# Kernel tuning notes

Hardware: AMD Instinct MI355X
Metric: run time of the kernel (lower is better)

Reference implementation:

```python
import jax, jax.numpy as jnp
import numpy as np


def setup_inputs() -> dict:
    key = jax.random.key(0)
    k1, k2, k3, k4 = jax.random.split(key, 4)
    B, T, C, H = 4, 4096, 1024, 64
    x = jax.random.normal(k1, (B, T, C), dtype=jnp.float32)
    Wq = jax.random.normal(k2, (C, H), dtype=jnp.float32) * (C ** -0.5)
    Wk = jax.random.normal(k3, (C, H), dtype=jnp.float32) * (C ** -0.5)
    Wv = jax.random.normal(k4, (C, H), dtype=jnp.float32) * (C ** -0.5)
    return {"x": x, "Wq": Wq, "Wk": Wk, "Wv": Wv}


def reference(x, Wq, Wk, Wv):
    B, T, C = x.shape
    q = jnp.einsum('btc,ch->bth', x, Wq)  # [B,T,H]
    k = jnp.einsum('btc,ch->bth', x, Wk)
    v = jnp.einsum('btc,ch->bth', x, Wv)
    # NOTE: original scales by C**0.5 (embed_dim), not head_size**0.5
    scale = jnp.asarray(C, x.dtype) ** 0.5
    wei = jnp.einsum('bth,bsh->bts', q, k) / scale  # [B,T,T]
    causal = jnp.tril(jnp.ones((T, T), dtype=bool))
    wei = jnp.where(causal, wei, -jnp.inf)
    wei = jax.nn.softmax(wei, axis=-1)  # dropout p=0.0 -> identity
    return jnp.einsum('bts,bsh->bth', wei, v)  # [B,T,H]
```

## Files before the change

### kernel.cpp

```cpp
#include <hip/hip_runtime.h>
#include <hip/hip_bf16.h>

typedef __bf16 bf16;
typedef __bf16 bf16x8 __attribute__((ext_vector_type(8)));
typedef __bf16 bf16x4 __attribute__((ext_vector_type(4)));
typedef float  f32x4  __attribute__((ext_vector_type(4)));

#define MFMA16(A, B, C) __builtin_amdgcn_mfma_f32_16x16x32_bf16((A), (B), (C), 0, 0, 0)

static constexpr int Bn = 4;
static constexpr int T  = 4096;
static constexpr int Cd = 1024;
static constexpr int H  = 64;
static constexpr int NG = 192;
static constexpr int CH = 8;
static constexpr int SLOTS_PER_B = 288;
static constexpr float QSCALE = 0.03125f;

__device__ inline void dma16(const void* g, void* l) {
    __builtin_amdgcn_global_load_lds(
        (const __attribute__((address_space(1))) unsigned int*)g,
        (__attribute__((address_space(3))) unsigned int*)l, 16, 0, 0);
}

__device__ inline bf16x8 cvt_bf16x8(float4 a, float4 b) {
    bf16x8 r;
    r[0] = (bf16)a.x; r[1] = (bf16)a.y; r[2] = (bf16)a.z; r[3] = (bf16)a.w;
    r[4] = (bf16)b.x; r[5] = (bf16)b.y; r[6] = (bf16)b.z; r[7] = (bf16)b.w;
    return r;
}

__global__ __launch_bounds__(256) void wt_kernel(const float* __restrict__ Wq,
                                                 const float* __restrict__ Wk,
                                                 const float* __restrict__ Wv,
                                                 bf16* __restrict__ Wt) {
    __shared__ float s[64][65];
    const int cb = blockIdx.x;
    const int m  = blockIdx.y;
    const float* W = (m == 0) ? Wq : (m == 1) ? Wk : Wv;
    for (int i = threadIdx.x; i < 64 * 64; i += 256) {
        const int c = i >> 6, h = i & 63;
        s[c][h] = W[(cb * 64 + c) * H + h];
    }
    __syncthreads();
    for (int i = threadIdx.x; i < 64 * 64; i += 256) {
        const int n = i >> 6, c = i & 63;
        Wt[(m * 64 + n) * Cd + cb * 64 + c] = (bf16)s[c][n];
    }
}

__global__ __launch_bounds__(256, 4) void proj_kernel(const float* __restrict__ x,
                                                      const bf16* __restrict__ Wt,
                                                      bf16* __restrict__ qw,
                                                      bf16* __restrict__ kw,
                                                      bf16* __restrict__ vtw) {
    const int tid  = threadIdx.x;
    const int lane = tid & 63;
    const int w    = tid >> 6;
    const int ml   = lane & 15;
    const int quad = lane >> 4;

    const long r0 = (long)blockIdx.x * 16;

    __shared__ float sX[2][16][64];

    const int drow = w * 4 + (lane >> 4);
    const int dchk = lane & 15;
    const float* gx = x + (r0 + drow) * Cd + ((dchk ^ drow) << 2);

    f32x4 acc[3];
    #pragma unroll
    for (int j = 0; j < 3; ++j) acc[j] = f32x4{0.f, 0.f, 0.f, 0.f};

    const bf16* wb = Wt + (long)(w * 48 + ml) * Cd + quad * 8;

    dma16(gx, &sX[0][w * 4][0]);
    __syncthreads();

    int buf = 0;
    for (int kb = 0; kb < Cd; kb += 64) {
        if (kb + 64 < Cd)
            dma16(gx + kb + 64, &sX[buf ^ 1][w * 4][0]);

        const bf16x8 w00 = *(const bf16x8*)(wb + kb);
        const bf16x8 w01 = *(const bf16x8*)(wb + 16 * Cd + kb);
        const bf16x8 w02 = *(const bf16x8*)(wb + 32 * Cd + kb);
        const bf16x8 w10 = *(const bf16x8*)(wb + kb + 32);
        const bf16x8 w11 = *(const bf16x8*)(wb + 16 * Cd + kb + 32);
        const bf16x8 w12 = *(const bf16x8*)(wb + 32 * Cd + kb + 32);

        const int c00 = (0 * 8 + quad * 2) ^ ml;
        const int c10 = (1 * 8 + quad * 2) ^ ml;
        const float4 lo0 = *(const float4*)&sX[buf][ml][c00 << 2];
        const float4 hi0 = *(const float4*)&sX[buf][ml][(c00 ^ 1) << 2];
        const float4 lo1 = *(const float4*)&sX[buf][ml][c10 << 2];
        const float4 hi1 = *(const float4*)&sX[buf][ml][(c10 ^ 1) << 2];
        const bf16x8 af0 = cvt_bf16x8(lo0, hi0);
        const bf16x8 af1 = cvt_bf16x8(lo1, hi1);

        acc[0] = MFMA16(af0, w00, acc[0]);
        acc[1] = MFMA16(af0, w01, acc[1]);
        acc[2] = MFMA16(af0, w02, acc[2]);
        acc[0] = MFMA16(af1, w10, acc[0]);
        acc[1] = MFMA16(af1, w11, acc[1]);
        acc[2] = MFMA16(af1, w12, acc[2]);

        __syncthreads();
        buf ^= 1;
    }

    const int b = (int)(r0 >> 12);
    const long rowb = r0 + quad * 4;
    const int  tloc = (int)(rowb & 4095);

    #pragma unroll
    for (int f = 0; f < 3; ++f) {
        const int base = w * 48 + f * 16;
        const int sel  = base >> 6;
        const int h    = (base & 63) + ml;
        if (sel == 0) {
            #pragma unroll
            for (int rr = 0; rr < 4; ++rr)
                qw[(rowb + rr) * H + h] = (bf16)(acc[f][rr] * QSCALE);
        } else if (sel == 1) {
            #pragma unroll
            for (int rr = 0; rr < 4; ++rr)
                kw[(rowb + rr) * H + h] = (bf16)acc[f][rr];
        } else {
            bf16x4 pv;
            #pragma unroll
            for (int rr = 0; rr < 4; ++rr) pv[rr] = (bf16)acc[f][rr];
            *(bf16x4*)(vtw + ((long)(b * H + h)) * T + tloc) = pv;
        }
    }
}

__global__ __launch_bounds__(256, 3) void attn_kernel(const bf16* __restrict__ qw,
                                                      const bf16* __restrict__ kw,
                                                      const bf16* __restrict__ vtw,
                                                      float* __restrict__ pO,
                                                      float* __restrict__ pL) {
    const int qt = blockIdx.x;
    const int c  = blockIdx.y;
    const int b  = blockIdx.z;
    const int g  = qt >> 3, r = qt & 7;
    if (c > g) return;

    const int tid  = threadIdx.x;
    const int lane = tid & 63;
    const int w    = tid >> 6;
    const int ml   = lane & 15;
    const int quad = lane >> 4;
    const int mx   = ml & 7;

    __shared__ bf16 sK[2][64][64];
    __shared__ bf16 sVt[2][64][64];
    __shared__ bf16 sP[4][16][72];

    const int t0 = qt * 64;

    const bf16* q0 = qw + ((long)b * T + t0 + w * 16 + ml) * H;
    const bf16x8 aq0 = *(const bf16x8*)(q0 + quad * 8);
    const bf16x8 aq1 = *(const bf16x8*)(q0 + 32 + quad * 8);

    f32x4 O[4];
    #pragma unroll
    for (int ht = 0; ht < 4; ++ht) O[ht] = f32x4{0.f, 0.f, 0.f, 0.f};
    float lrow[4] = {0.f, 0.f, 0.f, 0.f};

    const int trow = t0 + w * 16 + quad * 4;
    const int jt0 = c * CH;
    const int jt1 = (c == g) ? qt + 1 : (c + 1) * CH;

    const int drow = w * 8 + (lane >> 3);
    const int dsw  = ((lane & 7) ^ (drow & 7)) << 3;
    const bf16* kbase = kw + (long)b * T * H;
    const bf16* vbase = vtw + (long)b * H * T;
    const long koffA = (long)drow * H + dsw;
    const long koffB = koffA + 32 * H;
    const long voffA = (long)drow * T + dsw;
    const long voffB = voffA + (long)32 * T;

    {
        const long ks0 = (long)jt0 * 64;
        dma16(kbase + ks0 * H + koffA, &sK[0][w * 8][0]);
        dma16(kbase + ks0 * H + koffB, &sK[0][32 + w * 8][0]);
        dma16(vbase + ks0 + voffA, &sVt[0][w * 8][0]);
        dma16(vbase + ks0 + voffB, &sVt[0][32 + w * 8][0]);
    }
    __syncthreads();

    int buf = 0;
    for (int jt = jt0; jt < jt1; ++jt) {
        if (jt + 1 < jt1) {
            const long ksn = (long)(jt + 1) * 64;
            dma16(kbase + ksn * H + koffA, &sK[buf ^ 1][w * 8][0]);
            dma16(kbase + ksn * H + koffB, &sK[buf ^ 1][32 + w * 8][0]);
            dma16(vbase + ksn + voffA, &sVt[buf ^ 1][w * 8][0]);
            dma16(vbase + ksn + voffB, &sVt[buf ^ 1][32 + w * 8][0]);
        }

        const int s0 = jt * 64;
        const bool diag = (jt == qt);
        #pragma unroll
        for (int nt = 0; nt < 4; ++nt) {
            f32x4 sacc = f32x4{0.f, 0.f, 0.f, 0.f};
            sacc = MFMA16(aq0, *(const bf16x8*)&sK[buf][nt * 16 + ml][(quad ^ mx) << 3], sacc);
            sacc = MFMA16(aq1, *(const bf16x8*)&sK[buf][nt * 16 + ml][((4 + quad) ^ mx) << 3], sacc);
            const int col = s0 + nt * 16 + ml;
            #pragma unroll
            for (int rr = 0; rr < 4; ++rr) {
                const float p = (diag && col > trow + rr) ? 0.f : __expf(sacc[rr]);
                lrow[rr] += p;
                sP[w][quad * 4 + rr][nt * 16 + ml] = (bf16)p;
            }
        }
        asm volatile("s_waitcnt lgkmcnt(0)" ::: "memory");

        #pragma unroll
        for (int ks = 0; ks < 2; ++ks) {
            const bf16x8 ap = *(const bf16x8*)&sP[w][ml][ks * 32 + quad * 8];
            #pragma unroll
            for (int ht = 0; ht < 4; ++ht)
                O[ht] = MFMA16(ap,
                    *(const bf16x8*)&sVt[buf][ht * 16 + ml][(((ks << 2) + quad) ^ mx) << 3],
                    O[ht]);
        }

        __syncthreads();
        buf ^= 1;
    }

    #pragma unroll
    for (int d = 1; d < 16; d <<= 1)
        #pragma unroll
        for (int rr = 0; rr < 4; ++rr)
            lrow[rr] += __shfl_xor(lrow[rr], d, 64);

    const long slot = (long)b * SLOTS_PER_B + (long)(g + 1) * (4 * g + r) + c;
    float* po = pO + slot * 4096 + (w * 16) * 64;
    #pragma unroll
    for (int ht = 0; ht < 4; ++ht)
        #pragma unroll
        for (int rr = 0; rr < 4; ++rr)
            po[(quad * 4 + rr) * 64 + ht * 16 + ml] = O[ht][rr];
    if (ml == 0) {
        #pragma unroll
        for (int rr = 0; rr < 4; ++rr)
            pL[slot * 64 + w * 16 + quad * 4 + rr] = lrow[rr];
    }
}

__global__ __launch_bounds__(256) void combine_kernel(const float* __restrict__ pO,
                                                      const float* __restrict__ pL,
                                                      float* __restrict__ out) {
    const int qt = blockIdx.x;
    const int b  = blockIdx.y;
    const int g  = qt >> 3, r = qt & 7;
    const int nch = g + 1;
    const long slot0 = (long)b * SLOTS_PER_B + (long)(g + 1) * (4 * g + r);

    const int tid = threadIdx.x;
    const int row = tid >> 2;
    const int q4  = tid & 3;

    f32x4 o[4];
    #pragma unroll
    for (int j = 0; j < 4; ++j) o[j] = f32x4{0.f, 0.f, 0.f, 0.f};
    float l = 0.f;

    for (int cc = 0; cc < nch; ++cc) {
        const float* po = pO + (slot0 + cc) * 4096 + row * 64 + q4 * 16;
        #pragma unroll
        for (int j = 0; j < 4; ++j) o[j] += *(const f32x4*)(po + j * 4);
        l += pL[(slot0 + cc) * 64 + row];
    }
    const float inv = 1.f / l;
    float* op = out + ((long)b * T + qt * 64 + row) * H + q4 * 16;
    #pragma unroll
    for (int j = 0; j < 4; ++j) {
        f32x4 v = o[j];
        v[0] *= inv; v[1] *= inv; v[2] *= inv; v[3] *= inv;
        *(f32x4*)(op + j * 4) = v;
    }
}

extern "C" void kernel_launch(void* const* d_in, const int* in_sizes, int n_in,
                              void* d_out, int out_size, void* d_ws, size_t ws_size,
                              hipStream_t stream) {
    const float* x  = (const float*)d_in[0];
    const float* Wq = (const float*)d_in[1];
    const float* Wk = (const float*)d_in[2];
    const float* Wv = (const float*)d_in[3];
    float* out = (float*)d_out;

    char* ws = (char*)d_ws;
    const size_t WT_BYTES = (size_t)NG * Cd * sizeof(bf16);
    const size_t QK_BYTES = (size_t)Bn * T * H * sizeof(bf16);
    const size_t PO_OFF   = WT_BYTES + 3 * QK_BYTES;
    const size_t PO_BYTES = (size_t)Bn * SLOTS_PER_B * 4096 * sizeof(float);
    bf16*  Wt  = (bf16*)ws;
    bf16*  qw  = (bf16*)(ws + WT_BYTES);
    bf16*  kw  = (bf16*)(ws + WT_BYTES + QK_BYTES);
    bf16*  vtw = (bf16*)(ws + WT_BYTES + 2 * QK_BYTES);
    float* pO  = (float*)(ws + PO_OFF);
    float* pL  = (float*)(ws + PO_OFF + PO_BYTES);

    wt_kernel<<<dim3(16, 3), dim3(256), 0, stream>>>(Wq, Wk, Wv, Wt);
    proj_kernel<<<dim3((Bn * T) / 16), dim3(256), 0, stream>>>(x, Wt, qw, kw, vtw);
    attn_kernel<<<dim3(T / 64, CH, Bn), dim3(256), 0, stream>>>(qw, kw, vtw, pO, pL);
    combine_kernel<<<dim3(T / 64, Bn), dim3(256), 0, stream>>>(pO, pL, out);
}
```

Baseline: 178.6 us.

## Stage projection weights in LDS and double the row tile per block

The projection kernel now processes 32 rows per block with 512 threads and arranges its eight waves as a 2x4 grid. Each K-step's bf16 weight slice is DMA'd into a swizzled, double-buffered LDS tile and shared across waves, replacing per-wave global loads of the weights. This is meant to cut redundant global/L2 traffic for the weights and halve the number of blocks that re-read them. In exchange it uses more LDS per block (about 65 KB), which may limit occupancy.

```diff
diff --git a/kernel.cpp b/kernel.cpp
--- a/kernel.cpp
+++ b/kernel.cpp
@@ -49,7 +49,7 @@
     }
 }
 
-__global__ __launch_bounds__(256, 4) void proj_kernel(const float* __restrict__ x,
+__global__ __launch_bounds__(512, 4) void proj_kernel(const float* __restrict__ x,
                                                       const bf16* __restrict__ Wt,
                                                       bf16* __restrict__ qw,
                                                       bf16* __restrict__ kw,
@@ -57,65 +57,69 @@
     const int tid  = threadIdx.x;
     const int lane = tid & 63;
     const int w    = tid >> 6;
+    const int wr   = w >> 2;
+    const int wc   = w & 3;
     const int ml   = lane & 15;
     const int quad = lane >> 4;
 
-    const long r0 = (long)blockIdx.x * 16;
-
-    __shared__ float sX[2][16][64];
-
-    const int drow = w * 4 + (lane >> 4);
-    const int dchk = lane & 15;
-    const float* gx = x + (r0 + drow) * Cd + ((dchk ^ drow) << 2);
+    const long r0 = (long)blockIdx.x * 32;
+
+    __shared__ float sX[2][32][64];
+    __shared__ bf16  sW[2][192][64];
+
+    const int xrow = w * 4 + (lane >> 4);
+    const float* gx = x + (r0 + xrow) * Cd + (((lane & 15) ^ (xrow & 15)) << 2);
+    const int wchunk = ((lane & 7) ^ (lane >> 3)) << 3;
+    const bf16* gw0 = Wt + (long)(w * 24 + 0 + (lane >> 3)) * Cd + wchunk;
+    const bf16* gw1 = Wt + (long)(w * 24 + 8 + (lane >> 3)) * Cd + wchunk;
+    const bf16* gw2 = Wt + (long)(w * 24 + 16 + (lane >> 3)) * Cd + wchunk;
 
     f32x4 acc[3];
     #pragma unroll
     for (int j = 0; j < 3; ++j) acc[j] = f32x4{0.f, 0.f, 0.f, 0.f};
 
-    const bf16* wb = Wt + (long)(w * 48 + ml) * Cd + quad * 8;
-
     dma16(gx, &sX[0][w * 4][0]);
+    dma16(gw0, &sW[0][w * 24 + 0][0]);
+    dma16(gw1, &sW[0][w * 24 + 8][0]);
+    dma16(gw2, &sW[0][w * 24 + 16][0]);
     __syncthreads();
+
+    const int arow = wr * 16 + ml;
+    const int brow0 = wc * 48 + ml;
+    const int bsw = ml & 7;
 
     int buf = 0;
     for (int kb = 0; kb < Cd; kb += 64) {
-        if (kb + 64 < Cd)
+        if (kb + 64 < Cd) {
             dma16(gx + kb + 64, &sX[buf ^ 1][w * 4][0]);
-
-        const bf16x8 w00 = *(const bf16x8*)(wb + kb);
-        const bf16x8 w01 = *(const bf16x8*)(wb + 16 * Cd + kb);
-        const bf16x8 w02 = *(const bf16x8*)(wb + 32 * Cd + kb);
-        const bf16x8 w10 = *(const bf16x8*)(wb + kb + 32);
-        const bf16x8 w11 = *(const bf16x8*)(wb + 16 * Cd + kb + 32);
-        const bf16x8 w12 = *(const bf16x8*)(wb + 32 * Cd + kb + 32);
-
-        const int c00 = (0 * 8 + quad * 2) ^ ml;
-        const int c10 = (1 * 8 + quad * 2) ^ ml;
-        const float4 lo0 = *(const float4*)&sX[buf][ml][c00 << 2];
-        const float4 hi0 = *(const float4*)&sX[buf][ml][(c00 ^ 1) << 2];
-        const float4 lo1 = *(const float4*)&sX[buf][ml][c10 << 2];
-        const float4 hi1 = *(const float4*)&sX[buf][ml][(c10 ^ 1) << 2];
-        const bf16x8 af0 = cvt_bf16x8(lo0, hi0);
-        const bf16x8 af1 = cvt_bf16x8(lo1, hi1);
-
-        acc[0] = MFMA16(af0, w00, acc[0]);
-        acc[1] = MFMA16(af0, w01, acc[1]);
-        acc[2] = MFMA16(af0, w02, acc[2]);
-        acc[0] = MFMA16(af1, w10, acc[0]);
-        acc[1] = MFMA16(af1, w11, acc[1]);
-        acc[2] = MFMA16(af1, w12, acc[2]);
+            dma16(gw0 + kb + 64, &sW[buf ^ 1][w * 24 + 0][0]);
+            dma16(gw1 + kb + 64, &sW[buf ^ 1][w * 24 + 8][0]);
+            dma16(gw2 + kb + 64, &sW[buf ^ 1][w * 24 + 16][0]);
+        }
+
+        #pragma unroll
+        for (int ks = 0; ks < 2; ++ks) {
+            const int ca = (ks * 8 + quad * 2) ^ ml;
+            const float4 lo = *(const float4*)&sX[buf][arow][ca << 2];
+            const float4 hi = *(const float4*)&sX[buf][arow][(ca ^ 1) << 2];
+            const bf16x8 af = cvt_bf16x8(lo, hi);
+            const int cb0 = (ks * 4 + quad) ^ bsw;
+            acc[0] = MFMA16(af, *(const bf16x8*)&sW[buf][brow0 + 0][cb0 << 3], acc[0]);
+            acc[1] = MFMA16(af, *(const bf16x8*)&sW[buf][brow0 + 16][cb0 << 3], acc[1]);
+            acc[2] = MFMA16(af, *(const bf16x8*)&sW[buf][brow0 + 32][cb0 << 3], acc[2]);
+        }
 
         __syncthreads();
         buf ^= 1;
     }
 
     const int b = (int)(r0 >> 12);
-    const long rowb = r0 + quad * 4;
+    const long rowb = r0 + wr * 16 + quad * 4;
     const int  tloc = (int)(rowb & 4095);
 
     #pragma unroll
     for (int f = 0; f < 3; ++f) {
-        const int base = w * 48 + f * 16;
+        const int base = wc * 48 + f * 16;
         const int sel  = base >> 6;
         const int h    = (base & 63) + ml;
         if (sel == 0) {
@@ -307,7 +311,7 @@
     float* pL  = (float*)(ws + PO_OFF + PO_BYTES);
 
     wt_kernel<<<dim3(16, 3), dim3(256), 0, stream>>>(Wq, Wk, Wv, Wt);
-    proj_kernel<<<dim3((Bn * T) / 16), dim3(256), 0, stream>>>(x, Wt, qw, kw, vtw);
+    proj_kernel<<<dim3((Bn * T) / 32), dim3(512), 0, stream>>>(x, Wt, qw, kw, vtw);
     attn_kernel<<<dim3(T / 64, CH, Bn), dim3(256), 0, stream>>>(qw, kw, vtw, pO, pL);
     combine_kernel<<<dim3(T / 64, Bn), dim3(256), 0, stream>>>(pO, pL, out);
 }
```

After: 153.4 us. 14.1% less time.
